# Kernel tuning notes

Hardware: AMD Instinct MI355X
Metric: run time of the kernel (lower is better)

Reference implementation:

```python
import jax, jax.numpy as jnp
import numpy as np

EMBED = 1024
HEADS = 16
HEAD_DIM = EMBED // HEADS


def setup_inputs() -> dict:
    key = jax.random.key(0)
    ks = jax.random.split(key, 8)
    B, S, D = 4, 2048, EMBED
    s = 1.0 / np.sqrt(D)
    return {
        "values": jax.random.normal(ks[0], (B, S, D), jnp.float32),
        "keys": jax.random.normal(ks[1], (B, S, D), jnp.float32),
        "query": jax.random.normal(ks[2], (B, S, D), jnp.float32),
        "Wv": jax.random.normal(ks[3], (D, D), jnp.float32) * s,
        "Wk": jax.random.normal(ks[4], (D, D), jnp.float32) * s,
        "Wq": jax.random.normal(ks[5], (D, D), jnp.float32) * s,
        "Wo": jax.random.normal(ks[6], (D, D), jnp.float32) * s,
        "bo": jax.random.normal(ks[7], (D,), jnp.float32) * 0.01,
    }


def reference(values, keys, query, Wv, Wk, Wq, Wo, bo):
    N, Lq, D = query.shape
    Lk = keys.shape[1]
    Lv = values.shape[1]
    # torch Linear: y = x @ W.T
    v = (values @ Wv.T).reshape(N, Lv, HEADS, HEAD_DIM)
    k = (keys @ Wk.T).reshape(N, Lk, HEADS, HEAD_DIM)
    q = (query @ Wq.T).reshape(N, Lq, HEADS, HEAD_DIM)
    energy = jnp.einsum('nqhd,nkhd->nhqk', q, k)
    # NOTE: module scales by 1/sqrt(embed_size), not 1/sqrt(head_dim)
    attn = jax.nn.softmax(energy / jnp.sqrt(jnp.float32(D)), axis=3)
    out = jnp.einsum('nhql,nlhd->nqhd', attn, v).reshape(N, Lq, D)
    return out @ Wo.T + bo
```

## Files before the change

### kernel.cpp

```cpp
#include <hip/hip_runtime.h>
#include <cstdint>
#include <cstddef>


typedef unsigned short ushortT;
typedef __bf16 bf16x8 __attribute__((ext_vector_type(8)));
typedef float f32x4 __attribute__((ext_vector_type(4)));
typedef unsigned short us4 __attribute__((ext_vector_type(4)));
typedef unsigned short us8 __attribute__((ext_vector_type(8)));

#define S_LEN 2048
#define NB 4
#define NH 16
#define HD 64
#define DMODEL 1024
#define MTOT 8192
#define WSZ 1048576

#define AS1 __attribute__((address_space(1)))
#define AS3 __attribute__((address_space(3)))

__device__ __forceinline__ ushortT f2b(float f) {
  unsigned x = __builtin_bit_cast(unsigned, f);
  x += 0x7fffu + ((x >> 16) & 1u);
  return (ushortT)(x >> 16);
}

__device__ __forceinline__ unsigned rne_pack(unsigned lo, unsigned hi) {
  lo += 0x7fffu + ((lo >> 16) & 1u);
  hi += 0x7fffu + ((hi >> 16) & 1u);
  return __builtin_amdgcn_perm(hi, lo, 0x07060302u);
}

__device__ __forceinline__ f32x4 mfma_bf16(bf16x8 a, bf16x8 b, f32x4 c) {
  return __builtin_amdgcn_mfma_f32_16x16x32_bf16(a, b, c, 0, 0, 0);
}

__device__ __forceinline__ void gl2lds16(const ushortT* g, ushortT* l) {
  __builtin_amdgcn_global_load_lds((const AS1 void*)g, (AS3 void*)l, 16, 0, 0);
}

__global__ __launch_bounds__(256) void convert_w_kernel(
    const float* __restrict__ wq, const float* __restrict__ wk,
    const float* __restrict__ wv, const float* __restrict__ wo,
    ushortT* __restrict__ dst) {
  const float* s;
  switch (blockIdx.y) {
    case 0: s = wq; break;
    case 1: s = wk; break;
    case 2: s = wv; break;
    default: s = wo; break;
  }
  ushortT* d = dst + (size_t)blockIdx.y * WSZ;
  const size_t i = ((size_t)blockIdx.x * 256 + threadIdx.x) * 8;
  uint4 w0 = *(const uint4*)(s + i);
  uint4 w1 = *(const uint4*)(s + i + 4);
  uint4 pk;
  pk.x = rne_pack(w0.x, w0.y);
  pk.y = rne_pack(w0.z, w0.w);
  pk.z = rne_pack(w1.x, w1.y);
  pk.w = rne_pack(w1.z, w1.w);
  *(uint4*)(d + i) = pk;
}

template <int VT_MODE, bool A_F32, bool OUT_F32, bool HAS_BIAS>
__device__ __forceinline__ void gemm_bt_tile(const void* __restrict__ A,
                                             const ushortT* __restrict__ W,
                                             const float* __restrict__ bias,
                                             void* __restrict__ C, float oscale,
                                             ushortT* As, ushortT* Bs) {
  constexpr int K = 1024, N = 1024;
  const int tid = threadIdx.x;
  const int wave = tid >> 6, lane = tid & 63, quad = lane >> 4, l16 = lane & 15;
  const int wm = wave & 1, wn = wave >> 1;
  const int bx = blockIdx.x, by = blockIdx.y;

  const size_t Aoff = (size_t)by * 128 * K;
  const ushortT* Wb = W + (size_t)bx * 128 * K;

  const f32x4 fz = {0.f, 0.f, 0.f, 0.f};
  f32x4 acc[4][4];
#pragma unroll
  for (int mi = 0; mi < 4; mi++)
#pragma unroll
    for (int ni = 0; ni < 4; ni++) acc[mi][ni] = fz;

  for (int kt = 0; kt < K; kt += 32) {
    __syncthreads();
#pragma unroll
    for (int i = 0; i < 2; ++i) {
      const int cb = (wave * 2 + i) * 64;
      const int c = cb + lane;
      const int m = c >> 2, ko = c & 3;
      gl2lds16(Wb + (size_t)m * K + kt + ko * 8, Bs + (size_t)cb * 8);
    }
    if (A_F32) {
#pragma unroll
      for (int j = 0; j < 2; ++j) {
        const int c = tid + j * 256;
        const int m = c >> 2, ko = c & 3;
        const float* ap = (const float*)A + Aoff + (size_t)m * K + kt + ko * 8;
        uint4 w0 = *(const uint4*)ap;
        uint4 w1 = *(const uint4*)(ap + 4);
        uint4 pk;
        pk.x = rne_pack(w0.x, w0.y);
        pk.y = rne_pack(w0.z, w0.w);
        pk.z = rne_pack(w1.x, w1.y);
        pk.w = rne_pack(w1.z, w1.w);
        *(uint4*)(As + (size_t)c * 8) = pk;
      }
    } else {
#pragma unroll
      for (int i = 0; i < 2; ++i) {
        const int cb = (wave * 2 + i) * 64;
        const int c = cb + lane;
        const int m = c >> 2, ko = c & 3;
        gl2lds16((const ushortT*)A + Aoff + (size_t)m * K + kt + ko * 8,
                 As + (size_t)cb * 8);
      }
    }
    __syncthreads();

    bf16x8 af[4], bfr[4];
#pragma unroll
    for (int mi = 0; mi < 4; mi++)
      af[mi] = *(const bf16x8*)(As + (wm * 64 + mi * 16 + l16) * 32 + quad * 8);
#pragma unroll
    for (int ni = 0; ni < 4; ni++)
      bfr[ni] = *(const bf16x8*)(Bs + (wn * 64 + ni * 16 + l16) * 32 + quad * 8);
#pragma unroll
    for (int mi = 0; mi < 4; mi++)
#pragma unroll
      for (int ni = 0; ni < 4; ni++)
        acc[mi][ni] = mfma_bf16(af[mi], bfr[ni], acc[mi][ni]);
  }

#pragma unroll
  for (int mi = 0; mi < 4; mi++) {
    const int row0 = by * 128 + wm * 64 + mi * 16 + quad * 4;
#pragma unroll
    for (int ni = 0; ni < 4; ni++) {
      const int col = bx * 128 + wn * 64 + ni * 16 + l16;
      const float bv = HAS_BIAS ? bias[col] : 0.f;
      if (VT_MODE == 0) {
#pragma unroll
        for (int i = 0; i < 4; i++) {
          const size_t idx = (size_t)(row0 + i) * N + col;
          const float val = acc[mi][ni][i] * oscale + bv;
          if (OUT_F32)
            ((float*)C)[idx] = val;
          else
            ((ushortT*)C)[idx] = f2b(val);
        }
      } else {
        const int h = col >> 6, dd = col & 63;
        const int bb = row0 >> 11, s0 = row0 & (S_LEN - 1);
        us4 pk;
#pragma unroll
        for (int i = 0; i < 4; i++) pk[i] = f2b(acc[mi][ni][i]);
        *(us4*)((ushortT*)C + ((size_t)((bb * NH + h) * HD + dd) << 11) + s0) =
            pk;
      }
    }
  }
}

__global__ __launch_bounds__(256) void qkv_proj_kernel(
    const float* __restrict__ vals, const float* __restrict__ keys,
    const float* __restrict__ qry, const ushortT* __restrict__ wcat,
    ushortT* __restrict__ qb, ushortT* __restrict__ kb,
    ushortT* __restrict__ vtb) {
  __shared__ alignas(16) ushortT As[128 * 32];
  __shared__ alignas(16) ushortT Bs[128 * 32];
  const int z = blockIdx.z;
  const float QSC = 1.44269504088896f / 32.0f;
  if (z == 0)
    gemm_bt_tile<0, true, false, false>(qry, wcat, nullptr, qb, QSC, As, Bs);
  else if (z == 1)
    gemm_bt_tile<0, true, false, false>(keys, wcat + WSZ, nullptr, kb, 1.0f,
                                        As, Bs);
  else
    gemm_bt_tile<1, true, false, false>(vals, wcat + 2 * WSZ, nullptr, vtb,
                                        1.0f, As, Bs);
}

__global__ __launch_bounds__(256) void out_proj_kernel(
    const ushortT* __restrict__ ain, const ushortT* __restrict__ wo,
    const float* __restrict__ bo, float* __restrict__ out) {
  __shared__ alignas(16) ushortT As[128 * 32];
  __shared__ alignas(16) ushortT Bs[128 * 32];
  gemm_bt_tile<0, false, true, true>(ain, wo, bo, out, 1.0f, As, Bs);
}

__global__ __launch_bounds__(256) void attn_kernel(
    const ushortT* __restrict__ qb, const ushortT* __restrict__ kb,
    const ushortT* __restrict__ vtb, ushortT* __restrict__ ab) {
  __shared__ alignas(16) ushortT Vts[64 * 136];
  __shared__ alignas(16) ushortT KPs[128 * 136];
  ushortT* Ks = KPs;
  ushortT* Ps = KPs;

  const int tid = threadIdx.x;
  const int wave = tid >> 6, lane = tid & 63, quad = lane >> 4, l16 = lane & 15;
  const int qt = blockIdx.x, bh = blockIdx.y, b = bh >> 4, h = bh & 15;

  bf16x8 qf[2][2];
#pragma unroll
  for (int mi = 0; mi < 2; mi++)
#pragma unroll
    for (int kq = 0; kq < 2; kq++) {
      const int qrow = qt * 128 + wave * 32 + mi * 16 + l16;
      qf[mi][kq] = *(const bf16x8*)(qb + (size_t)(b * S_LEN + qrow) * DMODEL +
                                    h * HD + kq * 32 + quad * 8);
    }

  const f32x4 fz = {0.f, 0.f, 0.f, 0.f};
  f32x4 osum[2][4];
#pragma unroll
  for (int mi = 0; mi < 2; mi++)
#pragma unroll
    for (int ni = 0; ni < 4; ni++) osum[mi][ni] = fz;
  float lsum[2][4];
#pragma unroll
  for (int mi = 0; mi < 2; mi++)
#pragma unroll
    for (int i = 0; i < 4; i++) lsum[mi][i] = 0.f;

  us8 kreg[4], vreg[4];
  auto issue_loads = [&](int t) {
#pragma unroll
    for (int p = 0; p < 4; p++) {
      const int r = (tid >> 3) + p * 32, c = (tid & 7) * 8;
      kreg[p] = *(const us8*)(kb + (size_t)(b * S_LEN + t * 128 + r) * DMODEL +
                              h * HD + c);
    }
#pragma unroll
    for (int p = 0; p < 4; p++) {
      const int r = (tid >> 4) + p * 16, c = (tid & 15) * 8;
      vreg[p] = *(const us8*)(vtb + (size_t)((b * NH + h) * HD + r) * S_LEN +
                              t * 128 + c);
    }
  };
  issue_loads(0);

  for (int t = 0; t < 16; ++t) {
    __syncthreads();
#pragma unroll
    for (int p = 0; p < 4; p++) {
      const int r = (tid >> 3) + p * 32, c = (tid & 7) * 8;
      *(us8*)(Ks + r * 72 + c) = kreg[p];
    }
#pragma unroll
    for (int p = 0; p < 4; p++) {
      const int r = (tid >> 4) + p * 16, c = (tid & 15) * 8;
      *(us8*)(Vts + r * 136 + c) = vreg[p];
    }
    if (t < 15) issue_loads(t + 1);
    __syncthreads();

    f32x4 sacc[2][8];
#pragma unroll
    for (int mi = 0; mi < 2; mi++)
#pragma unroll
      for (int ni = 0; ni < 8; ni++) sacc[mi][ni] = fz;
#pragma unroll
    for (int kq = 0; kq < 2; kq++)
#pragma unroll
      for (int ni = 0; ni < 8; ni++) {
        bf16x8 kf =
            *(const bf16x8*)(Ks + (ni * 16 + l16) * 72 + kq * 32 + quad * 8);
#pragma unroll
        for (int mi = 0; mi < 2; mi++)
          sacc[mi][ni] = mfma_bf16(qf[mi][kq], kf, sacc[mi][ni]);
      }
    __syncthreads();

#pragma unroll
    for (int mi = 0; mi < 2; mi++)
#pragma unroll
      for (int i = 0; i < 4; i++) {
        const int prow = wave * 32 + mi * 16 + quad * 4 + i;
        float rs = 0.f;
#pragma unroll
        for (int ni = 0; ni < 8; ni++) {
          const float p = __builtin_amdgcn_exp2f(sacc[mi][ni][i]);
          rs += p;
          Ps[prow * 136 + ni * 16 + l16] = f2b(p);
        }
        lsum[mi][i] += rs;
      }
    __syncthreads();

#pragma unroll
    for (int ks = 0; ks < 4; ks++) {
      bf16x8 pa[2];
#pragma unroll
      for (int mi = 0; mi < 2; mi++)
        pa[mi] = *(const bf16x8*)(Ps + (wave * 32 + mi * 16 + l16) * 136 +
                                  ks * 32 + quad * 8);
#pragma unroll
      for (int ni = 0; ni < 4; ni++) {
        bf16x8 vf =
            *(const bf16x8*)(Vts + (ni * 16 + l16) * 136 + ks * 32 + quad * 8);
#pragma unroll
        for (int mi = 0; mi < 2; mi++)
          osum[mi][ni] = mfma_bf16(pa[mi], vf, osum[mi][ni]);
      }
    }
  }

#pragma unroll
  for (int mi = 0; mi < 2; mi++)
#pragma unroll
    for (int i = 0; i < 4; i++) {
      float s = lsum[mi][i];
#pragma unroll
      for (int d = 1; d < 16; d <<= 1) s += __shfl_xor(s, d, 64);
      const float inv = 1.0f / s;
      const int orow = qt * 128 + wave * 32 + mi * 16 + quad * 4 + i;
#pragma unroll
      for (int ni = 0; ni < 4; ni++)
        ab[(size_t)(b * S_LEN + orow) * DMODEL + h * HD + ni * 16 + l16] =
            f2b(osum[mi][ni][i] * inv);
    }
}

extern "C" void kernel_launch(void* const* d_in, const int* in_sizes, int n_in,
                              void* d_out, int out_size, void* d_ws,
                              size_t ws_size, hipStream_t stream) {
  const float* vals = (const float*)d_in[0];
  const float* keys = (const float*)d_in[1];
  const float* qry = (const float*)d_in[2];
  const float* Wv = (const float*)d_in[3];
  const float* Wk = (const float*)d_in[4];
  const float* Wq = (const float*)d_in[5];
  const float* Wo = (const float*)d_in[6];
  const float* bo = (const float*)d_in[7];
  float* out = (float*)d_out;

  ushortT* ws = (ushortT*)d_ws;
  const size_t E = (size_t)MTOT * DMODEL;
  ushortT* qbuf = ws;
  ushortT* kbuf = ws + E;
  ushortT* vtb = ws + 2 * E;
  ushortT* wcat = ws + 3 * E;
  ushortT* abuf = qbuf;

  dim3 blk(256, 1, 1);
  convert_w_kernel<<<dim3(512, 4), blk, 0, stream>>>(Wq, Wk, Wv, Wo, wcat);
  qkv_proj_kernel<<<dim3(8, 64, 3), blk, 0, stream>>>(vals, keys, qry, wcat,
                                                      qbuf, kbuf, vtb);
  attn_kernel<<<dim3(16, 64, 1), blk, 0, stream>>>(qbuf, kbuf, vtb, abuf);
  out_proj_kernel<<<dim3(8, 64, 1), blk, 0, stream>>>(abuf, wcat + 3 * WSZ, bo,
                                                      out);
}
```

Baseline: 400.5 us.

## Keep softmax probabilities in registers via transposed QK^T and fp16 PV MFMA

```diff
diff --git a/kernel.cpp b/kernel.cpp
--- a/kernel.cpp
+++ b/kernel.cpp
@@ -5,7 +5,10 @@
 
 typedef unsigned short ushortT;
 typedef __bf16 bf16x8 __attribute__((ext_vector_type(8)));
+typedef _Float16 f16x4 __attribute__((ext_vector_type(4)));
+typedef _Float16 f16x2 __attribute__((ext_vector_type(2)));
 typedef float f32x4 __attribute__((ext_vector_type(4)));
+typedef unsigned int u32x2 __attribute__((ext_vector_type(2)));
 typedef unsigned short us4 __attribute__((ext_vector_type(4)));
 typedef unsigned short us8 __attribute__((ext_vector_type(8)));
 
@@ -34,6 +37,9 @@
 
 __device__ __forceinline__ f32x4 mfma_bf16(bf16x8 a, bf16x8 b, f32x4 c) {
   return __builtin_amdgcn_mfma_f32_16x16x32_bf16(a, b, c, 0, 0, 0);
+}
+__device__ __forceinline__ f32x4 mfma16_f16(f16x4 a, f16x4 b, f32x4 c) {
+  return __builtin_amdgcn_mfma_f32_16x16x16f16(a, b, c, 0, 0, 0);
 }
 
 __device__ __forceinline__ void gl2lds16(const ushortT* g, ushortT* l) {
@@ -73,7 +79,7 @@
   const int tid = threadIdx.x;
   const int wave = tid >> 6, lane = tid & 63, quad = lane >> 4, l16 = lane & 15;
   const int wm = wave & 1, wn = wave >> 1;
-  const int bx = blockIdx.x, by = blockIdx.y;
+  const int by = blockIdx.x, bx = blockIdx.y;
 
   const size_t Aoff = (size_t)by * 128 * K;
   const ushortT* Wb = W + (size_t)bx * 128 * K;
@@ -155,10 +161,12 @@
       } else {
         const int h = col >> 6, dd = col & 63;
         const int bb = row0 >> 11, s0 = row0 & (S_LEN - 1);
-        us4 pk;
-#pragma unroll
-        for (int i = 0; i < 4; i++) pk[i] = f2b(acc[mi][ni][i]);
-        *(us4*)((ushortT*)C + ((size_t)((bb * NH + h) * HD + dd) << 11) + s0) =
+        u32x2 pk;
+        pk[0] = __builtin_bit_cast(
+            unsigned, __builtin_amdgcn_cvt_pkrtz(acc[mi][ni][0], acc[mi][ni][1]));
+        pk[1] = __builtin_bit_cast(
+            unsigned, __builtin_amdgcn_cvt_pkrtz(acc[mi][ni][2], acc[mi][ni][3]));
+        *(u32x2*)((ushortT*)C + ((size_t)((bb * NH + h) * HD + dd) << 11) + s0) =
             pk;
       }
     }
@@ -195,14 +203,12 @@
 __global__ __launch_bounds__(256) void attn_kernel(
     const ushortT* __restrict__ qb, const ushortT* __restrict__ kb,
     const ushortT* __restrict__ vtb, ushortT* __restrict__ ab) {
+  __shared__ alignas(16) ushortT Ks[128 * 72];
   __shared__ alignas(16) ushortT Vts[64 * 136];
-  __shared__ alignas(16) ushortT KPs[128 * 136];
-  ushortT* Ks = KPs;
-  ushortT* Ps = KPs;
 
   const int tid = threadIdx.x;
   const int wave = tid >> 6, lane = tid & 63, quad = lane >> 4, l16 = lane & 15;
-  const int qt = blockIdx.x, bh = blockIdx.y, b = bh >> 4, h = bh & 15;
+  const int bh = blockIdx.x, qt = blockIdx.y, b = bh >> 4, h = bh & 15;
 
   bf16x8 qf[2][2];
 #pragma unroll
@@ -215,16 +221,12 @@
     }
 
   const f32x4 fz = {0.f, 0.f, 0.f, 0.f};
-  f32x4 osum[2][4];
-#pragma unroll
-  for (int mi = 0; mi < 2; mi++)
-#pragma unroll
-    for (int ni = 0; ni < 4; ni++) osum[mi][ni] = fz;
-  float lsum[2][4];
-#pragma unroll
-  for (int mi = 0; mi < 2; mi++)
-#pragma unroll
-    for (int i = 0; i < 4; i++) lsum[mi][i] = 0.f;
+  f32x4 osum[4][2];
+#pragma unroll
+  for (int ni = 0; ni < 4; ni++)
+#pragma unroll
+    for (int mi = 0; mi < 2; mi++) osum[ni][mi] = fz;
+  float lsum[2] = {0.f, 0.f};
 
   us8 kreg[4], vreg[4];
   auto issue_loads = [&](int t) {
@@ -258,71 +260,74 @@
     if (t < 15) issue_loads(t + 1);
     __syncthreads();
 
-    f32x4 sacc[2][8];
-#pragma unroll
-    for (int mi = 0; mi < 2; mi++)
-#pragma unroll
-      for (int ni = 0; ni < 8; ni++) sacc[mi][ni] = fz;
-#pragma unroll
-    for (int kq = 0; kq < 2; kq++)
-#pragma unroll
-      for (int ni = 0; ni < 8; ni++) {
-        bf16x8 kf =
-            *(const bf16x8*)(Ks + (ni * 16 + l16) * 72 + kq * 32 + quad * 8);
-#pragma unroll
-        for (int mi = 0; mi < 2; mi++)
-          sacc[mi][ni] = mfma_bf16(qf[mi][kq], kf, sacc[mi][ni]);
-      }
-    __syncthreads();
-
-#pragma unroll
-    for (int mi = 0; mi < 2; mi++)
-#pragma unroll
-      for (int i = 0; i < 4; i++) {
-        const int prow = wave * 32 + mi * 16 + quad * 4 + i;
-        float rs = 0.f;
-#pragma unroll
-        for (int ni = 0; ni < 8; ni++) {
-          const float p = __builtin_amdgcn_exp2f(sacc[mi][ni][i]);
-          rs += p;
-          Ps[prow * 136 + ni * 16 + l16] = f2b(p);
+#pragma unroll
+    for (int h2 = 0; h2 < 2; ++h2) {
+      f32x4 sacc[4][2];
+#pragma unroll
+      for (int mt = 0; mt < 4; mt++)
+#pragma unroll
+        for (int mi = 0; mi < 2; mi++) sacc[mt][mi] = fz;
+#pragma unroll
+      for (int kq = 0; kq < 2; kq++)
+#pragma unroll
+        for (int mt = 0; mt < 4; mt++) {
+          bf16x8 kf = *(const bf16x8*)(Ks + ((h2 * 4 + mt) * 16 + l16) * 72 +
+                                       kq * 32 + quad * 8);
+#pragma unroll
+          for (int mi = 0; mi < 2; mi++)
+            sacc[mt][mi] = mfma_bf16(kf, qf[mi][kq], sacc[mt][mi]);
         }
-        lsum[mi][i] += rs;
-      }
-    __syncthreads();
-
-#pragma unroll
-    for (int ks = 0; ks < 4; ks++) {
-      bf16x8 pa[2];
-#pragma unroll
-      for (int mi = 0; mi < 2; mi++)
-        pa[mi] = *(const bf16x8*)(Ps + (wave * 32 + mi * 16 + l16) * 136 +
-                                  ks * 32 + quad * 8);
-#pragma unroll
-      for (int ni = 0; ni < 4; ni++) {
-        bf16x8 vf =
-            *(const bf16x8*)(Vts + (ni * 16 + l16) * 136 + ks * 32 + quad * 8);
-#pragma unroll
-        for (int mi = 0; mi < 2; mi++)
-          osum[mi][ni] = mfma_bf16(pa[mi], vf, osum[mi][ni]);
-      }
-    }
-  }
-
-#pragma unroll
-  for (int mi = 0; mi < 2; mi++)
-#pragma unroll
-    for (int i = 0; i < 4; i++) {
-      float s = lsum[mi][i];
-#pragma unroll
-      for (int d = 1; d < 16; d <<= 1) s += __shfl_xor(s, d, 64);
-      const float inv = 1.0f / s;
-      const int orow = qt * 128 + wave * 32 + mi * 16 + quad * 4 + i;
-#pragma unroll
-      for (int ni = 0; ni < 4; ni++)
-        ab[(size_t)(b * S_LEN + orow) * DMODEL + h * HD + ni * 16 + l16] =
-            f2b(osum[mi][ni][i] * inv);
-    }
+
+      u32x2 pf[4][2];
+#pragma unroll
+      for (int mt = 0; mt < 4; mt++)
+#pragma unroll
+        for (int mi = 0; mi < 2; mi++) {
+          const float e0 = __builtin_amdgcn_exp2f(sacc[mt][mi][0]);
+          const float e1 = __builtin_amdgcn_exp2f(sacc[mt][mi][1]);
+          const float e2 = __builtin_amdgcn_exp2f(sacc[mt][mi][2]);
+          const float e3 = __builtin_amdgcn_exp2f(sacc[mt][mi][3]);
+          lsum[mi] += (e0 + e1) + (e2 + e3);
+          pf[mt][mi][0] =
+              __builtin_bit_cast(unsigned, __builtin_amdgcn_cvt_pkrtz(e0, e1));
+          pf[mt][mi][1] =
+              __builtin_bit_cast(unsigned, __builtin_amdgcn_cvt_pkrtz(e2, e3));
+        }
+
+#pragma unroll
+      for (int s = 0; s < 4; ++s)
+#pragma unroll
+        for (int ni = 0; ni < 4; ni++) {
+          f16x4 vf = *(const f16x4*)(Vts + (ni * 16 + l16) * 136 +
+                                     (h2 * 4 + s) * 16 + quad * 4);
+#pragma unroll
+          for (int mi = 0; mi < 2; mi++)
+            osum[ni][mi] =
+                mfma16_f16(vf, __builtin_bit_cast(f16x4, pf[s][mi]), osum[ni][mi]);
+        }
+    }
+  }
+
+#pragma unroll
+  for (int mi = 0; mi < 2; mi++) {
+    float s = lsum[mi];
+    s += __shfl_xor(s, 16, 64);
+    s += __shfl_xor(s, 32, 64);
+    lsum[mi] = 1.0f / s;
+  }
+
+#pragma unroll
+  for (int mi = 0; mi < 2; mi++) {
+    const int qrow = qt * 128 + wave * 32 + mi * 16 + l16;
+#pragma unroll
+    for (int ni = 0; ni < 4; ni++) {
+      us4 pk;
+#pragma unroll
+      for (int i = 0; i < 4; i++) pk[i] = f2b(osum[ni][mi][i] * lsum[mi]);
+      *(us4*)(ab + (size_t)(b * S_LEN + qrow) * DMODEL + h * HD + ni * 16 +
+              quad * 4) = pk;
+    }
+  }
 }
 
 extern "C" void kernel_launch(void* const* d_in, const int* in_sizes, int n_in,
@@ -348,9 +353,9 @@
 
   dim3 blk(256, 1, 1);
   convert_w_kernel<<<dim3(512, 4), blk, 0, stream>>>(Wq, Wk, Wv, Wo, wcat);
-  qkv_proj_kernel<<<dim3(8, 64, 3), blk, 0, stream>>>(vals, keys, qry, wcat,
+  qkv_proj_kernel<<<dim3(64, 8, 3), blk, 0, stream>>>(vals, keys, qry, wcat,
                                                       qbuf, kbuf, vtb);
-  attn_kernel<<<dim3(16, 64, 1), blk, 0, stream>>>(qbuf, kbuf, vtb, abuf);
-  out_proj_kernel<<<dim3(8, 64, 1), blk, 0, stream>>>(abuf, wcat + 3 * WSZ, bo,
-                                                      out);
-}
+  attn_kernel<<<dim3(64, 16), blk, 0, stream>>>(qbuf, kbuf, vtb, abuf);
+  out_proj_kernel<<<dim3(64, 8), blk, 0, stream>>>(abuf, wcat + 3 * WSZ, bo,
+                                                   out);
+}
```

After: 363.6 us. 1.1x faster.
